# Kernel tuning notes

Hardware: AMD Instinct MI355X
Metric: run time of the kernel (lower is better)

## Reference

```python
import jax, jax.numpy as jnp
import numpy as np

N, E, G, H, NF, EF, GF, L = 204800, 600000, 3200, 128, 16, 5, 8, 6
EPS = 1e-5


def setup_inputs() -> dict:
    key = jax.random.key(0)
    ks = jax.random.split(key, 24)
    s = 0.05
    inp = {
        'x': jax.random.normal(ks[0], (N, NF), jnp.float32),
        'edge_index': jax.random.randint(ks[1], (2, E), 0, N, jnp.int32),
        'edge_attr': jax.random.normal(ks[2], (E, EF), jnp.float32),
        'global_features': jax.random.normal(ks[3], (G, GF), jnp.float32),
        'batch': (jnp.arange(N, dtype=jnp.int32) // (N // G)),
        'node_w': jax.random.normal(ks[4], (NF, H), jnp.float32) * s,
        'node_b': jnp.zeros((H,), jnp.float32),
        'edge_w': jax.random.normal(ks[5], (EF, H), jnp.float32) * s,
        'edge_b': jnp.zeros((H,), jnp.float32),
        'rel_w': jax.random.normal(ks[6], (L, H, H), jnp.float32) * s,
        'rel_b': jnp.zeros((L, H), jnp.float32),
        'root_w': jax.random.normal(ks[7], (L, H, H), jnp.float32) * s,
        'bn_gamma': jnp.ones((L, H), jnp.float32),
        'bn_beta': jnp.zeros((L, H), jnp.float32),
        'gate_w1': jax.random.normal(ks[8], (H, H), jnp.float32) * s,
        'gate_b1': jnp.zeros((H,), jnp.float32),
        'gate_w2': jax.random.normal(ks[9], (H, 1), jnp.float32) * s,
        'gate_b2': jnp.zeros((1,), jnp.float32),
        'gf_w': jax.random.normal(ks[10], (GF, H), jnp.float32) * s,
        'gf_b': jnp.zeros((H,), jnp.float32),
        'gi_w': jax.random.normal(ks[11], (2 * H, H), jnp.float32) * s,
        'gi_b': jnp.zeros((H,), jnp.float32),
    }
    return inp


def reference(x, edge_index, edge_attr, global_features, batch,
              node_w, node_b, edge_w, edge_b,
              rel_w, rel_b, root_w, bn_gamma, bn_beta,
              gate_w1, gate_b1, gate_w2, gate_b2,
              gf_w, gf_b, gi_w, gi_b):
    n = x.shape[0]
    src, dst = edge_index[0], edge_index[1]
    h = x @ node_w + node_b                       # [N,H]
    ea = edge_attr @ edge_w + edge_b              # [E,H]
    for i in range(L):
        identity = h
        msg = h[src] * ea                         # [E,H] gather + edge weighting
        agg = jax.ops.segment_sum(msg, dst, num_segments=n)  # scatter-add
        h2 = agg @ rel_w[i] + rel_b[i] + h @ root_w[i]        # GraphConv
        mean = jnp.mean(h2, axis=0)
        var = jnp.mean(jnp.square(h2 - mean), axis=0)         # biased (BN train)
        h2 = (h2 - mean) * jax.lax.rsqrt(var + EPS) * bn_gamma[i] + bn_beta[i]
        h = jax.nn.relu(h2 + identity)
    # GlobalAttention: segment softmax over gate scores, weighted sum of h
    gate = (jax.nn.relu(h @ gate_w1 + gate_b1) @ gate_w2 + gate_b2)[:, 0]  # [N]
    m = jax.ops.segment_max(gate, batch, num_segments=G)
    e = jnp.exp(gate - m[batch])
    ssum = jax.ops.segment_sum(e, batch, num_segments=G)
    alpha = e / ssum[batch]
    pooled = jax.ops.segment_sum(alpha[:, None] * h, batch, num_segments=G)  # [G,H]
    gf = global_features @ gf_w + gf_b
    global_embedding = jnp.concatenate([pooled, gf], axis=1) @ gi_w + gi_b
    return (h, global_embedding)
```

## Files before the change

### kernel.cpp

```cpp
#include <hip/hip_runtime.h>
#include <math.h>

#define N_NODES 204800
#define N_EDGES 600000
#define N_GRAPH 3200
#define H 128
#define NF 16
#define EF 5
#define GF 8
#define LAYERS 6
#define SEG 64
#define EPSV 1e-5f
#define NB_SCAN 800
#define NBLK 3200

typedef __attribute__((ext_vector_type(8))) short bf16x8;
typedef __attribute__((ext_vector_type(4))) float f32x4;

__device__ inline float bf2f(unsigned int u) {
    return __builtin_bit_cast(float, u << 16);
}
__device__ inline unsigned short f2bf(float f) {
    unsigned int u = __builtin_bit_cast(unsigned int, f);
    u += 0x7fffu + ((u >> 16) & 1u);
    return (unsigned short)(u >> 16);
}
__device__ inline float uif(unsigned int u) { return __builtin_bit_cast(float, u); }

__global__ __launch_bounds__(256) void k_init_h(
    const float* __restrict__ x, const float* __restrict__ node_w,
    const float* __restrict__ node_b, unsigned short* __restrict__ hb)
{
    int idx = blockIdx.x * 256 + threadIdx.x;
    int n = idx >> 4, c0 = (idx & 15) * 8;
    const float4* xr = (const float4*)(x + (size_t)n * NF);
    float4 x0 = xr[0], x1 = xr[1], x2 = xr[2], x3 = xr[3];
    float xa[16] = {x0.x, x0.y, x0.z, x0.w, x1.x, x1.y, x1.z, x1.w,
                    x2.x, x2.y, x2.z, x2.w, x3.x, x3.y, x3.z, x3.w};
    float4 a0 = *(const float4*)(node_b + c0);
    float4 a1 = *(const float4*)(node_b + c0 + 4);
#pragma unroll
    for (int k = 0; k < NF; ++k) {
        float xv = xa[k];
        float4 w0 = *(const float4*)(node_w + k * H + c0);
        float4 w1 = *(const float4*)(node_w + k * H + c0 + 4);
        a0.x += xv * w0.x; a0.y += xv * w0.y; a0.z += xv * w0.z; a0.w += xv * w0.w;
        a1.x += xv * w1.x; a1.y += xv * w1.y; a1.z += xv * w1.z; a1.w += xv * w1.w;
    }
    uint4 pk;
    pk.x = (unsigned int)f2bf(a0.x) | ((unsigned int)f2bf(a0.y) << 16);
    pk.y = (unsigned int)f2bf(a0.z) | ((unsigned int)f2bf(a0.w) << 16);
    pk.z = (unsigned int)f2bf(a1.x) | ((unsigned int)f2bf(a1.y) << 16);
    pk.w = (unsigned int)f2bf(a1.z) | ((unsigned int)f2bf(a1.w) << 16);
    *(uint4*)(hb + (size_t)n * H + c0) = pk;
}

__global__ __launch_bounds__(64) void k_wpack(
    const float* __restrict__ relw, const float* __restrict__ rootw,
    unsigned short* __restrict__ wp)
{
    int bid = blockIdx.x;
    int i = bid >> 6, f = bid & 63;
    int nb = f >> 3, ks = f & 7;
    int l = threadIdx.x;
    const float* src = (ks < 4) ? (relw + (size_t)i * H * H) : (rootw + (size_t)i * H * H);
    int ksl = ks & 3;
    int col = nb * 16 + (l & 15);
    int kbase = ksl * 32 + (l >> 4) * 8;
    unsigned short tmp[8];
#pragma unroll
    for (int m = 0; m < 8; ++m)
        tmp[m] = f2bf(src[(size_t)(kbase + m) * H + col]);
    *(uint4*)(wp + ((size_t)bid * 64 + l) * 8) = *(uint4*)tmp;
}

__global__ __launch_bounds__(64) void k_wpack_gate(
    const float* __restrict__ gw1, unsigned short* __restrict__ gwp)
{
    int bid = blockIdx.x;
    int nb = bid >> 2, ks = bid & 3;
    int l = threadIdx.x;
    int col = nb * 16 + (l & 15);
    int kbase = ks * 32 + (l >> 4) * 8;
    unsigned short tmp[8];
#pragma unroll
    for (int m = 0; m < 8; ++m)
        tmp[m] = f2bf(gw1[(size_t)(kbase + m) * H + col]);
    *(uint4*)(gwp + ((size_t)bid * 64 + l) * 8) = *(uint4*)tmp;
}

__global__ __launch_bounds__(256) void k_deg(const int* __restrict__ ei, int* __restrict__ deg)
{
    int e = blockIdx.x * 256 + threadIdx.x;
    if (e < N_EDGES) atomicAdd(&deg[ei[N_EDGES + e]], 1);
}

__global__ __launch_bounds__(256) void k_scan1(
    const int* __restrict__ deg, int* __restrict__ rowtmp, int* __restrict__ bsum)
{
    __shared__ int sh[256];
    int t = threadIdx.x;
    int i = blockIdx.x * 256 + t;
    int v = deg[i];
    sh[t] = v;
    __syncthreads();
    for (int off = 1; off < 256; off <<= 1) {
        int a = (t >= off) ? sh[t - off] : 0;
        __syncthreads();
        sh[t] += a;
        __syncthreads();
    }
    rowtmp[i] = sh[t] - v;
    if (t == 255) bsum[blockIdx.x] = sh[255];
}

__global__ void k_scan2(int* __restrict__ bsum, int* __restrict__ boff)
{
    __shared__ int sh[256];
    __shared__ int carry;
    int t = threadIdx.x;
    if (t == 0) carry = 0;
    __syncthreads();
    for (int base = 0; base < NB_SCAN; base += 256) {
        int i = base + t;
        int v = (i < NB_SCAN) ? bsum[i] : 0;
        sh[t] = v;
        __syncthreads();
        for (int off = 1; off < 256; off <<= 1) {
            int a = (t >= off) ? sh[t - off] : 0;
            __syncthreads();
            sh[t] += a;
            __syncthreads();
        }
        if (i < NB_SCAN) boff[i] = carry + sh[t] - v;
        __syncthreads();
        if (t == 0) carry += sh[255];
        __syncthreads();
    }
}

__global__ __launch_bounds__(256) void k_scan3(
    const int* __restrict__ rowtmp, const int* __restrict__ boff,
    int* __restrict__ rowptr, int* __restrict__ cursor)
{
    int i = blockIdx.x * 256 + threadIdx.x;
    int r = rowtmp[i] + boff[blockIdx.x];
    rowptr[i] = r;
    cursor[i] = r;
    if (i == 0) rowptr[N_NODES] = N_EDGES;
}

__global__ __launch_bounds__(256) void k_scatter(
    const int* __restrict__ ei, const float* __restrict__ eattr,
    int* __restrict__ cursor, uint4* __restrict__ recs)
{
    int e = blockIdx.x * 256 + threadIdx.x;
    if (e >= N_EDGES) return;
    int d = ei[N_EDGES + e];
    const float* ar = eattr + (size_t)e * EF;
    float c0 = ar[0], c1 = ar[1], c2 = ar[2], c3 = ar[3], c4 = ar[4];
    int pos = atomicAdd(&cursor[d], 1);
    uint4 q0, q1;
    q0.x = (unsigned int)ei[e];
    q0.y = __builtin_bit_cast(unsigned int, c0);
    q0.z = __builtin_bit_cast(unsigned int, c1);
    q0.w = __builtin_bit_cast(unsigned int, c2);
    q1.x = __builtin_bit_cast(unsigned int, c3);
    q1.y = __builtin_bit_cast(unsigned int, c4);
    q1.z = 0; q1.w = 0;
    recs[2 * (size_t)pos]     = q0;
    recs[2 * (size_t)pos + 1] = q1;
}

#define EDGE_ONE(q0, q1, A0, A1)                                               \
    {                                                                          \
        unsigned int hv = *(const unsigned int*)(hb + (size_t)(int)(q0).x * H + 2 * l); \
        float ea0 = eb2.x, ea1 = eb2.y;                                        \
        float c0 = uif((q0).y), c1 = uif((q0).z), c2 = uif((q0).w);            \
        float c3 = uif((q1).x), c4 = uif((q1).y);                              \
        ea0 += c0 * ew2[0].x + c1 * ew2[1].x + c2 * ew2[2].x + c3 * ew2[3].x + c4 * ew2[4].x; \
        ea1 += c0 * ew2[0].y + c1 * ew2[1].y + c2 * ew2[2].y + c3 * ew2[3].y + c4 * ew2[4].y; \
        A0 += bf2f(hv & 0xffffu) * ea0;                                        \
        A1 += bf2f(hv >> 16) * ea1;                                            \
    }

__global__ __launch_bounds__(256) void k_agg(
    const int* __restrict__ rowptr, const uint4* __restrict__ recs,
    const float* __restrict__ edge_w, const float* __restrict__ edge_b,
    const unsigned short* __restrict__ hb, unsigned short* __restrict__ aggb)
{
    int w = threadIdx.x >> 6, l = threadIdx.x & 63;
    int n = blockIdx.x * 8 + w * 2;
    float2 ew2[EF];
#pragma unroll
    for (int k = 0; k < EF; ++k) ew2[k] = ((const float2*)(edge_w + k * H))[l];
    float2 eb2 = ((const float2*)edge_b)[l];

    int jA = rowptr[n], eA = rowptr[n + 1];
    int jB = eA,        eB = rowptr[n + 2];
    float a0 = 0.f, a1 = 0.f, b0 = 0.f, b1 = 0.f;

    while (jA + 2 <= eA && jB + 2 <= eB) {
        uint4 qa0 = recs[2 * jA],     qa1 = recs[2 * jA + 1];
        uint4 qb0 = recs[2 * jA + 2], qb1 = recs[2 * jA + 3];
        uint4 qc0 = recs[2 * jB],     qc1 = recs[2 * jB + 1];
        uint4 qd0 = recs[2 * jB + 2], qd1 = recs[2 * jB + 3];
        EDGE_ONE(qa0, qa1, a0, a1);
        EDGE_ONE(qb0, qb1, a0, a1);
        EDGE_ONE(qc0, qc1, b0, b1);
        EDGE_ONE(qd0, qd1, b0, b1);
        jA += 2; jB += 2;
    }
    while (jA + 2 <= eA) {
        uint4 qa0 = recs[2 * jA],     qa1 = recs[2 * jA + 1];
        uint4 qb0 = recs[2 * jA + 2], qb1 = recs[2 * jA + 3];
        EDGE_ONE(qa0, qa1, a0, a1);
        EDGE_ONE(qb0, qb1, a0, a1);
        jA += 2;
    }
    if (jA < eA) {
        uint4 qa0 = recs[2 * jA], qa1 = recs[2 * jA + 1];
        EDGE_ONE(qa0, qa1, a0, a1);
    }
    while (jB + 2 <= eB) {
        uint4 qc0 = recs[2 * jB],     qc1 = recs[2 * jB + 1];
        uint4 qd0 = recs[2 * jB + 2], qd1 = recs[2 * jB + 3];
        EDGE_ONE(qc0, qc1, b0, b1);
        EDGE_ONE(qd0, qd1, b0, b1);
        jB += 2;
    }
    if (jB < eB) {
        uint4 qc0 = recs[2 * jB], qc1 = recs[2 * jB + 1];
        EDGE_ONE(qc0, qc1, b0, b1);
    }

    unsigned int pka = (unsigned int)f2bf(a0) | ((unsigned int)f2bf(a1) << 16);
    unsigned int pkb = (unsigned int)f2bf(b0) | ((unsigned int)f2bf(b1) << 16);
    *(unsigned int*)(aggb + (size_t)n * H + 2 * l)       = pka;
    *(unsigned int*)(aggb + (size_t)(n + 1) * H + 2 * l) = pkb;
}

__global__ __launch_bounds__(256) void k_gemm_mfma(
    const unsigned short* __restrict__ aggb,
    const unsigned short* __restrict__ hb,
    const unsigned short* __restrict__ wp,
    const float* __restrict__ relb,
    unsigned short* __restrict__ h2b,
    float* __restrict__ pbuf)
{
    __shared__ unsigned short smA[64 * 128];
    __shared__ unsigned short smH[64 * 128];
    int tid = threadIdx.x;
    int w = tid >> 6, l = tid & 63;
    int bid = blockIdx.x;
    int n0 = bid * 64;
    int lr = l & 15, hi = l >> 4;

    const char* aggp = (const char*)(aggb + (size_t)n0 * H);
    const char* hbp  = (const char*)(hb  + (size_t)n0 * H);
    char* sA = (char*)smA;
    char* sH = (char*)smH;
#pragma unroll
    for (int i = 0; i < 4; ++i) {
        int o = (i * 256 + tid) * 16;
        int row = o >> 8;
        int col = o & 255;
        int scol = col ^ ((row & 7) << 4);
        uint4 va = *(const uint4*)(aggp + o);
        uint4 vh = *(const uint4*)(hbp + o);
        *(uint4*)(sA + row * 256 + scol) = va;
        *(uint4*)(sH + row * 256 + scol) = vh;
    }
    __syncthreads();

    f32x4 acc[4][2];
#pragma unroll
    for (int rb = 0; rb < 4; ++rb) {
        acc[rb][0] = (f32x4){0.f, 0.f, 0.f, 0.f};
        acc[rb][1] = (f32x4){0.f, 0.f, 0.f, 0.f};
    }

    const bf16x8* wv = (const bf16x8*)wp;
#pragma unroll
    for (int ks = 0; ks < 4; ++ks) {
        bf16x8 b0 = wv[((2 * w + 0) * 8 + ks) * 64 + l];
        bf16x8 b1 = wv[((2 * w + 1) * 8 + ks) * 64 + l];
#pragma unroll
        for (int rb = 0; rb < 4; ++rb) {
            int r = rb * 16 + lr;
            int bc = (ks * 64 + hi * 16) ^ ((r & 7) << 4);
            bf16x8 a = *(const bf16x8*)(sA + r * 256 + bc);
            acc[rb][0] = __builtin_amdgcn_mfma_f32_16x16x32_bf16(a, b0, acc[rb][0], 0, 0, 0);
            acc[rb][1] = __builtin_amdgcn_mfma_f32_16x16x32_bf16(a, b1, acc[rb][1], 0, 0, 0);
        }
    }
#pragma unroll
    for (int ks = 0; ks < 4; ++ks) {
        bf16x8 b0 = wv[((2 * w + 0) * 8 + 4 + ks) * 64 + l];
        bf16x8 b1 = wv[((2 * w + 1) * 8 + 4 + ks) * 64 + l];
#pragma unroll
        for (int rb = 0; rb < 4; ++rb) {
            int r = rb * 16 + lr;
            int bc = (ks * 64 + hi * 16) ^ ((r & 7) << 4);
            bf16x8 a = *(const bf16x8*)(sH + r * 256 + bc);
            acc[rb][0] = __builtin_amdgcn_mfma_f32_16x16x32_bf16(a, b0, acc[rb][0], 0, 0, 0);
            acc[rb][1] = __builtin_amdgcn_mfma_f32_16x16x32_bf16(a, b1, acc[rb][1], 0, 0, 0);
        }
    }

#pragma unroll
    for (int nbl = 0; nbl < 2; ++nbl) {
        int col = w * 32 + nbl * 16 + lr;
        float bs = relb[col];
        float csum = 0.f, csq = 0.f;
#pragma unroll
        for (int rb = 0; rb < 4; ++rb) {
#pragma unroll
            for (int jj = 0; jj < 4; ++jj) {
                float v = acc[rb][nbl][jj] + bs;
                h2b[(size_t)(n0 + rb * 16 + hi * 4 + jj) * H + col] = f2bf(v);
                csum += v; csq += v * v;
            }
        }
        csum += __shfl_xor(csum, 16); csum += __shfl_xor(csum, 32);
        csq  += __shfl_xor(csq, 16);  csq  += __shfl_xor(csq, 32);
        if (hi == 0) {
            pbuf[(size_t)col * NBLK + bid]         = csum;
            pbuf[(size_t)(128 + col) * NBLK + bid] = csq;
        }
    }
}

__global__ __launch_bounds__(256) void k_red(
    const float* __restrict__ pbuf, const float* __restrict__ gamma,
    const float* __restrict__ beta, float* __restrict__ stats)
{
    __shared__ float sh[8];
    int c = blockIdx.x;
    int t = threadIdx.x;
    float s = 0.f, q = 0.f;
    const float* ps = pbuf + (size_t)c * NBLK;
    const float* pq = pbuf + (size_t)(128 + c) * NBLK;
    for (int i = t; i < NBLK; i += 256) { s += ps[i]; q += pq[i]; }
#pragma unroll
    for (int off = 32; off >= 1; off >>= 1) {
        s += __shfl_xor(s, off);
        q += __shfl_xor(q, off);
    }
    if ((t & 63) == 0) { sh[t >> 6] = s; sh[4 + (t >> 6)] = q; }
    __syncthreads();
    if (t == 0) {
        float S = sh[0] + sh[1] + sh[2] + sh[3];
        float Q = sh[4] + sh[5] + sh[6] + sh[7];
        float mean = S / (float)N_NODES;
        float var = fmaxf(Q / (float)N_NODES - mean * mean, 0.f);
        float scale = gamma[c] * rsqrtf(var + EPSV);
        stats[c] = scale;
        stats[128 + c] = beta[c] - mean * scale;
    }
}

template<bool LAST>
__global__ __launch_bounds__(256) void k_bn_apply(
    const unsigned short* __restrict__ h2b, const float* __restrict__ stats,
    unsigned short* __restrict__ hb, float* __restrict__ h)
{
    __shared__ float ssc[H], ssh[H];
    int tid = threadIdx.x;
    if (tid < H) {
        ssc[tid] = stats[tid];
        ssh[tid] = stats[128 + tid];
    }
    __syncthreads();
    size_t base = ((size_t)blockIdx.x * 256 + tid) * 8;
    int c = (int)(base & 127);
    uint4 hv2 = *(const uint4*)(h2b + base);
    uint4 hvp = *(const uint4*)(hb + base);
    unsigned int u2[4] = {hv2.x, hv2.y, hv2.z, hv2.w};
    unsigned int up[4] = {hvp.x, hvp.y, hvp.z, hvp.w};
    float o[8];
#pragma unroll
    for (int k = 0; k < 4; ++k) {
        float vlo = bf2f(u2[k] & 0xffffu), vhi = bf2f(u2[k] >> 16);
        float plo = bf2f(up[k] & 0xffffu), phi = bf2f(up[k] >> 16);
        o[2 * k]     = fmaxf(vlo * ssc[c + 2 * k]     + ssh[c + 2 * k]     + plo, 0.f);
        o[2 * k + 1] = fmaxf(vhi * ssc[c + 2 * k + 1] + ssh[c + 2 * k + 1] + phi, 0.f);
    }
    uint4 pk;
    pk.x = (unsigned int)f2bf(o[0]) | ((unsigned int)f2bf(o[1]) << 16);
    pk.y = (unsigned int)f2bf(o[2]) | ((unsigned int)f2bf(o[3]) << 16);
    pk.z = (unsigned int)f2bf(o[4]) | ((unsigned int)f2bf(o[5]) << 16);
    pk.w = (unsigned int)f2bf(o[6]) | ((unsigned int)f2bf(o[7]) << 16);
    *(uint4*)(hb + base) = pk;
    if (LAST) {
        *(float4*)(h + base)     = make_float4(o[0], o[1], o[2], o[3]);
        *(float4*)(h + base + 4) = make_float4(o[4], o[5], o[6], o[7]);
    }
}

__global__ __launch_bounds__(256) void k_gate_pool(
    const unsigned short* __restrict__ hb, const float* __restrict__ h,
    const unsigned short* __restrict__ gwp,
    const float* __restrict__ b1, const float* __restrict__ w2,
    const float* __restrict__ b2, float* __restrict__ pooled)
{
    __shared__ float Red[256];
    __shared__ float al[64];
    int tid = threadIdx.x;
    int w = tid >> 6, l = tid & 63;
    int lr = l & 15, hi = l >> 4;
    int g = blockIdx.x;
    int n0 = g * SEG;

    f32x4 acc[4][2];
#pragma unroll
    for (int rb = 0; rb < 4; ++rb) {
        acc[rb][0] = (f32x4){0.f, 0.f, 0.f, 0.f};
        acc[rb][1] = (f32x4){0.f, 0.f, 0.f, 0.f};
    }
    const bf16x8* wv = (const bf16x8*)gwp;
#pragma unroll
    for (int ks = 0; ks < 4; ++ks) {
        bf16x8 bb0 = wv[((2 * w + 0) * 4 + ks) * 64 + l];
        bf16x8 bb1 = wv[((2 * w + 1) * 4 + ks) * 64 + l];
#pragma unroll
        for (int rb = 0; rb < 4; ++rb) {
            bf16x8 a = *(const bf16x8*)(hb + (size_t)(n0 + rb * 16 + lr) * H + ks * 32 + hi * 8);
            acc[rb][0] = __builtin_amdgcn_mfma_f32_16x16x32_bf16(a, bb0, acc[rb][0], 0, 0, 0);
            acc[rb][1] = __builtin_amdgcn_mfma_f32_16x16x32_bf16(a, bb1, acc[rb][1], 0, 0, 0);
        }
    }
    int col0 = w * 32 + lr, col1 = w * 32 + 16 + lr;
    float b10 = b1[col0], b11 = b1[col1];
    float w20 = w2[col0], w21 = w2[col1];
    float p[4][4];
#pragma unroll
    for (int rb = 0; rb < 4; ++rb)
#pragma unroll
        for (int jj = 0; jj < 4; ++jj) {
            float v0 = fmaxf(acc[rb][0][jj] + b10, 0.f);
            float v1 = fmaxf(acc[rb][1][jj] + b11, 0.f);
            float s = v0 * w20 + v1 * w21;
            s += __shfl_xor(s, 1); s += __shfl_xor(s, 2);
            s += __shfl_xor(s, 4); s += __shfl_xor(s, 8);
            p[rb][jj] = s;
        }
    if (lr == 0) {
#pragma unroll
        for (int rb = 0; rb < 4; ++rb)
#pragma unroll
            for (int jj = 0; jj < 4; ++jj)
                Red[w * 64 + rb * 16 + hi * 4 + jj] = p[rb][jj];
    }
    __syncthreads();
    if (tid < 64) {
        float gt = Red[tid] + Red[64 + tid] + Red[128 + tid] + Red[192 + tid] + b2[0];
        float m = gt;
#pragma unroll
        for (int off = 32; off >= 1; off >>= 1) m = fmaxf(m, __shfl_xor(m, off));
        float e = expf(gt - m);
        float s = e;
#pragma unroll
        for (int off = 32; off >= 1; off >>= 1) s += __shfl_xor(s, off);
        al[tid] = e / s;
    }
    __syncthreads();
    int c = tid & 127, half = tid >> 7;
    float pp = 0.f;
    const float* hbase = h + (size_t)n0 * H;
    for (int j = half * 32; j < half * 32 + 32; ++j)
        pp += al[j] * hbase[(size_t)j * H + c];
    Red[tid] = pp;
    __syncthreads();
    if (tid < 128) pooled[(size_t)g * H + tid] = Red[tid] + Red[128 + tid];
}

__global__ __launch_bounds__(128) void k_final(
    const float* __restrict__ pooled, const float* __restrict__ gfeat,
    const float* __restrict__ gf_w, const float* __restrict__ gf_b,
    const float* __restrict__ gi_w, const float* __restrict__ gi_b,
    float* __restrict__ out)
{
    int g = blockIdx.x, c = threadIdx.x;
    __shared__ float prow[H], gfs[H];
    prow[c] = pooled[(size_t)g * H + c];
    float gv = gf_b[c];
    const float* gr = gfeat + (size_t)g * GF;
#pragma unroll
    for (int k = 0; k < GF; ++k) gv += gr[k] * gf_w[k * H + c];
    gfs[c] = gv;
    __syncthreads();
    float acc = gi_b[c];
    for (int k = 0; k < H; ++k) acc += prow[k] * gi_w[k * H + c];
    for (int k = 0; k < H; ++k) acc += gfs[k] * gi_w[(H + k) * H + c];
    out[(size_t)N_NODES * H + (size_t)g * H + c] = acc;
}

extern "C" void kernel_launch(void* const* d_in, const int* in_sizes, int n_in,
                              void* d_out, int out_size, void* d_ws, size_t ws_size,
                              hipStream_t stream)
{
    const float* x       = (const float*)d_in[0];
    const int*   ei      = (const int*)d_in[1];
    const float* eattr   = (const float*)d_in[2];
    const float* gfeat   = (const float*)d_in[3];
    const float* node_w  = (const float*)d_in[5];
    const float* node_b  = (const float*)d_in[6];
    const float* edge_w  = (const float*)d_in[7];
    const float* edge_b  = (const float*)d_in[8];
    const float* rel_w   = (const float*)d_in[9];
    const float* rel_b   = (const float*)d_in[10];
    const float* root_w  = (const float*)d_in[11];
    const float* bn_g    = (const float*)d_in[12];
    const float* bn_b    = (const float*)d_in[13];
    const float* gate_w1 = (const float*)d_in[14];
    const float* gate_b1 = (const float*)d_in[15];
    const float* gate_w2 = (const float*)d_in[16];
    const float* gate_b2 = (const float*)d_in[17];
    const float* gf_w    = (const float*)d_in[18];
    const float* gf_b    = (const float*)d_in[19];
    const float* gi_w    = (const float*)d_in[20];
    const float* gi_b    = (const float*)d_in[21];

    float* h   = (float*)d_out;
    float* out = (float*)d_out;

    char* wsb = (char*)d_ws;
    size_t off = 0;
    auto take = [&](size_t bytes) -> char* {
        char* r = wsb + off;
        off = (off + bytes + 63) & ~(size_t)63;
        return r;
    };
    unsigned short* h2b  = (unsigned short*)take((size_t)N_NODES * H * 2);
    unsigned short* hb   = (unsigned short*)take((size_t)N_NODES * H * 2);
    unsigned short* aggb = (unsigned short*)take((size_t)N_NODES * H * 2);
    unsigned short* wpck = (unsigned short*)take((size_t)LAYERS * 32768 * 2);
    unsigned short* gwp  = (unsigned short*)take((size_t)16384 * 2);
    float* pbuf   = (float*)take((size_t)256 * NBLK * 4);
    float* stats  = (float*)take((size_t)256 * 4);
    float* pooled = (float*)take((size_t)N_GRAPH * H * 4);
    int*   deg    = (int*)take((size_t)N_NODES * 4);
    int*   rowptr = (int*)take((size_t)(N_NODES + 1) * 4);
    int*   cursor = (int*)take((size_t)N_NODES * 4);
    int*   bsum   = (int*)take((size_t)NB_SCAN * 4);
    int*   boff   = (int*)take((size_t)NB_SCAN * 4);
    uint4* recs   = (uint4*)take((size_t)N_EDGES * 32);
    int*   rowtmp = cursor;

    hipMemsetAsync(deg, 0, N_NODES * sizeof(int), stream);
    k_deg<<<(N_EDGES + 255) / 256, 256, 0, stream>>>(ei, deg);
    k_scan1<<<NB_SCAN, 256, 0, stream>>>(deg, rowtmp, bsum);
    k_scan2<<<1, 256, 0, stream>>>(bsum, boff);
    k_scan3<<<NB_SCAN, 256, 0, stream>>>(rowtmp, boff, rowptr, cursor);
    k_scatter<<<(N_EDGES + 255) / 256, 256, 0, stream>>>(ei, eattr, cursor, recs);
    k_wpack<<<LAYERS * 64, 64, 0, stream>>>(rel_w, root_w, wpck);
    k_wpack_gate<<<32, 64, 0, stream>>>(gate_w1, gwp);

    k_init_h<<<N_NODES * 16 / 256, 256, 0, stream>>>(x, node_w, node_b, hb);

    for (int i = 0; i < LAYERS; ++i) {
        k_agg<<<N_NODES / 8, 256, 0, stream>>>(rowptr, recs, edge_w, edge_b, hb, aggb);
        k_gemm_mfma<<<NBLK, 256, 0, stream>>>(
            aggb, hb, wpck + (size_t)i * 32768, rel_b + (size_t)i * H,
            h2b, pbuf);
        k_red<<<128, 256, 0, stream>>>(pbuf, bn_g + (size_t)i * H, bn_b + (size_t)i * H, stats);
        if (i < LAYERS - 1)
            k_bn_apply<false><<<N_NODES * H / 8 / 256, 256, 0, stream>>>(h2b, stats, hb, h);
        else
            k_bn_apply<true><<<N_NODES * H / 8 / 256, 256, 0, stream>>>(h2b, stats, hb, h);
    }

    k_gate_pool<<<N_GRAPH, 256, 0, stream>>>(hb, h, gwp, gate_b1, gate_w2, gate_b2, pooled);
    k_final<<<N_GRAPH, H, 0, stream>>>(pooled, gfeat, gf_w, gf_b, gi_w, gi_b, out);
}
```

Measured before the change: 1.037 ms.

## Process 8 nodes per wave as one edge stream; pool from bf16 h

```diff
diff --git a/kernel.cpp b/kernel.cpp
--- a/kernel.cpp
+++ b/kernel.cpp
@@ -172,16 +172,20 @@
     recs[2 * (size_t)pos + 1] = q1;
 }
 
-#define EDGE_ONE(q0, q1, A0, A1)                                               \
-    {                                                                          \
-        unsigned int hv = *(const unsigned int*)(hb + (size_t)(int)(q0).x * H + 2 * l); \
+#define FOLD(jj, q0, q1, hv)                                                   \
+    if ((jj) < jend) {                                                         \
+        while ((jj) >= nend) {                                                 \
+            *(unsigned int*)(aggb + (size_t)(n0 + cur) * H + 2 * l) =          \
+                (unsigned int)f2bf(a0) | ((unsigned int)f2bf(a1) << 16);       \
+            a0 = 0.f; a1 = 0.f; ++cur; nend = __shfl(rpv, cur + 1);            \
+        }                                                                      \
         float ea0 = eb2.x, ea1 = eb2.y;                                        \
         float c0 = uif((q0).y), c1 = uif((q0).z), c2 = uif((q0).w);            \
         float c3 = uif((q1).x), c4 = uif((q1).y);                              \
         ea0 += c0 * ew2[0].x + c1 * ew2[1].x + c2 * ew2[2].x + c3 * ew2[3].x + c4 * ew2[4].x; \
         ea1 += c0 * ew2[0].y + c1 * ew2[1].y + c2 * ew2[2].y + c3 * ew2[3].y + c4 * ew2[4].y; \
-        A0 += bf2f(hv & 0xffffu) * ea0;                                        \
-        A1 += bf2f(hv >> 16) * ea1;                                            \
+        a0 += bf2f((hv) & 0xffffu) * ea0;                                      \
+        a1 += bf2f((hv) >> 16) * ea1;                                          \
     }
 
 __global__ __launch_bounds__(256) void k_agg(
@@ -190,54 +194,40 @@
     const unsigned short* __restrict__ hb, unsigned short* __restrict__ aggb)
 {
     int w = threadIdx.x >> 6, l = threadIdx.x & 63;
-    int n = blockIdx.x * 8 + w * 2;
+    int n0 = (blockIdx.x * 4 + w) * 8;
     float2 ew2[EF];
 #pragma unroll
     for (int k = 0; k < EF; ++k) ew2[k] = ((const float2*)(edge_w + k * H))[l];
     float2 eb2 = ((const float2*)edge_b)[l];
 
-    int jA = rowptr[n], eA = rowptr[n + 1];
-    int jB = eA,        eB = rowptr[n + 2];
-    float a0 = 0.f, a1 = 0.f, b0 = 0.f, b1 = 0.f;
-
-    while (jA + 2 <= eA && jB + 2 <= eB) {
-        uint4 qa0 = recs[2 * jA],     qa1 = recs[2 * jA + 1];
-        uint4 qb0 = recs[2 * jA + 2], qb1 = recs[2 * jA + 3];
-        uint4 qc0 = recs[2 * jB],     qc1 = recs[2 * jB + 1];
-        uint4 qd0 = recs[2 * jB + 2], qd1 = recs[2 * jB + 3];
-        EDGE_ONE(qa0, qa1, a0, a1);
-        EDGE_ONE(qb0, qb1, a0, a1);
-        EDGE_ONE(qc0, qc1, b0, b1);
-        EDGE_ONE(qd0, qd1, b0, b1);
-        jA += 2; jB += 2;
-    }
-    while (jA + 2 <= eA) {
-        uint4 qa0 = recs[2 * jA],     qa1 = recs[2 * jA + 1];
-        uint4 qb0 = recs[2 * jA + 2], qb1 = recs[2 * jA + 3];
-        EDGE_ONE(qa0, qa1, a0, a1);
-        EDGE_ONE(qb0, qb1, a0, a1);
-        jA += 2;
-    }
-    if (jA < eA) {
-        uint4 qa0 = recs[2 * jA], qa1 = recs[2 * jA + 1];
-        EDGE_ONE(qa0, qa1, a0, a1);
-    }
-    while (jB + 2 <= eB) {
-        uint4 qc0 = recs[2 * jB],     qc1 = recs[2 * jB + 1];
-        uint4 qd0 = recs[2 * jB + 2], qd1 = recs[2 * jB + 3];
-        EDGE_ONE(qc0, qc1, b0, b1);
-        EDGE_ONE(qd0, qd1, b0, b1);
-        jB += 2;
-    }
-    if (jB < eB) {
-        uint4 qc0 = recs[2 * jB], qc1 = recs[2 * jB + 1];
-        EDGE_ONE(qc0, qc1, b0, b1);
-    }
-
-    unsigned int pka = (unsigned int)f2bf(a0) | ((unsigned int)f2bf(a1) << 16);
-    unsigned int pkb = (unsigned int)f2bf(b0) | ((unsigned int)f2bf(b1) << 16);
-    *(unsigned int*)(aggb + (size_t)n * H + 2 * l)       = pka;
-    *(unsigned int*)(aggb + (size_t)(n + 1) * H + 2 * l) = pkb;
+    int rpv = rowptr[n0 + (l < 9 ? l : 8)];
+    int jbeg = __shfl(rpv, 0), jend = __shfl(rpv, 8);
+    int cur = 0;
+    int nend = __shfl(rpv, 1);
+    float a0 = 0.f, a1 = 0.f;
+
+    for (int j = jbeg; j < jend; j += 4) {
+        int jc1 = min(j + 1, jend - 1);
+        int jc2 = min(j + 2, jend - 1);
+        int jc3 = min(j + 3, jend - 1);
+        uint4 qa0 = recs[2 * (size_t)j],   qa1 = recs[2 * (size_t)j + 1];
+        uint4 qb0 = recs[2 * (size_t)jc1], qb1 = recs[2 * (size_t)jc1 + 1];
+        uint4 qc0 = recs[2 * (size_t)jc2], qc1 = recs[2 * (size_t)jc2 + 1];
+        uint4 qd0 = recs[2 * (size_t)jc3], qd1 = recs[2 * (size_t)jc3 + 1];
+        unsigned int hva = *(const unsigned int*)(hb + (size_t)(int)qa0.x * H + 2 * l);
+        unsigned int hvb = *(const unsigned int*)(hb + (size_t)(int)qb0.x * H + 2 * l);
+        unsigned int hvc = *(const unsigned int*)(hb + (size_t)(int)qc0.x * H + 2 * l);
+        unsigned int hvd = *(const unsigned int*)(hb + (size_t)(int)qd0.x * H + 2 * l);
+        FOLD(j,     qa0, qa1, hva);
+        FOLD(j + 1, qb0, qb1, hvb);
+        FOLD(j + 2, qc0, qc1, hvc);
+        FOLD(j + 3, qd0, qd1, hvd);
+    }
+    while (cur < 8) {
+        *(unsigned int*)(aggb + (size_t)(n0 + cur) * H + 2 * l) =
+            (unsigned int)f2bf(a0) | ((unsigned int)f2bf(a1) << 16);
+        a0 = 0.f; a1 = 0.f; ++cur;
+    }
 }
 
 __global__ __launch_bounds__(256) void k_gemm_mfma(
@@ -399,12 +389,12 @@
 }
 
 __global__ __launch_bounds__(256) void k_gate_pool(
-    const unsigned short* __restrict__ hb, const float* __restrict__ h,
+    const unsigned short* __restrict__ hb,
     const unsigned short* __restrict__ gwp,
     const float* __restrict__ b1, const float* __restrict__ w2,
     const float* __restrict__ b2, float* __restrict__ pooled)
 {
-    __shared__ float Red[256];
+    __shared__ float Red[512];
     __shared__ float al[64];
     int tid = threadIdx.x;
     int w = tid >> 6, l = tid & 63;
@@ -465,14 +455,20 @@
         al[tid] = e / s;
     }
     __syncthreads();
-    int c = tid & 127, half = tid >> 7;
-    float pp = 0.f;
-    const float* hbase = h + (size_t)n0 * H;
-    for (int j = half * 32; j < half * 32 + 32; ++j)
-        pp += al[j] * hbase[(size_t)j * H + c];
-    Red[tid] = pp;
-    __syncthreads();
-    if (tid < 128) pooled[(size_t)g * H + tid] = Red[tid] + Red[128 + tid];
+    int cq = tid & 63, qd = tid >> 6;
+    float p0 = 0.f, p1 = 0.f;
+    const unsigned short* hbase = hb + (size_t)n0 * H;
+    for (int j = qd * 16; j < qd * 16 + 16; ++j) {
+        unsigned int hv = *(const unsigned int*)(hbase + (size_t)j * H + 2 * cq);
+        float a = al[j];
+        p0 += a * bf2f(hv & 0xffffu);
+        p1 += a * bf2f(hv >> 16);
+    }
+    Red[qd * 128 + 2 * cq]     = p0;
+    Red[qd * 128 + 2 * cq + 1] = p1;
+    __syncthreads();
+    if (tid < 128)
+        pooled[(size_t)g * H + tid] = Red[tid] + Red[128 + tid] + Red[256 + tid] + Red[384 + tid];
 }
 
 __global__ __launch_bounds__(128) void k_final(
@@ -560,7 +556,7 @@
     k_init_h<<<N_NODES * 16 / 256, 256, 0, stream>>>(x, node_w, node_b, hb);
 
     for (int i = 0; i < LAYERS; ++i) {
-        k_agg<<<N_NODES / 8, 256, 0, stream>>>(rowptr, recs, edge_w, edge_b, hb, aggb);
+        k_agg<<<N_NODES / 32, 256, 0, stream>>>(rowptr, recs, edge_w, edge_b, hb, aggb);
         k_gemm_mfma<<<NBLK, 256, 0, stream>>>(
             aggb, hb, wpck + (size_t)i * 32768, rel_b + (size_t)i * H,
             h2b, pbuf);
@@ -571,6 +567,6 @@
             k_bn_apply<true><<<N_NODES * H / 8 / 256, 256, 0, stream>>>(h2b, stats, hb, h);
     }
 
-    k_gate_pool<<<N_GRAPH, 256, 0, stream>>>(hb, h, gwp, gate_b1, gate_w2, gate_b2, pooled);
+    k_gate_pool<<<N_GRAPH, 256, 0, stream>>>(hb, gwp, gate_b1, gate_w2, gate_b2, pooled);
     k_final<<<N_GRAPH, H, 0, stream>>>(pooled, gfeat, gf_w, gf_b, gi_w, gi_b, out);
 }
```

New measurement: 975.3 us. 1.06x faster.
